# Kernel optimization log

Measured on AMD Instinct MI355X. Metric: run time of the kernel, lower is better.

The kernel has to match this reference:

```python
import jax, jax.numpy as jnp
import numpy as np

N, E, T, IN, H, OUT = 100000, 800000, 8, 3, 32, 64


def _lstm_dir(pre, Whh, bhh, reverse):
    # pre: [T, E, 4H] precomputed input contribution (x @ W_ih^T + b_ih)
    Hh = Whh.shape[1]

    def step(carry, xt):
        h, c = carry
        g = xt + h @ Whh.T + bhh  # [E, 4H], pytorch gate order i,f,g,o
        i = jax.nn.sigmoid(g[:, :Hh])
        f = jax.nn.sigmoid(g[:, Hh:2 * Hh])
        gg = jnp.tanh(g[:, 2 * Hh:3 * Hh])
        o = jax.nn.sigmoid(g[:, 3 * Hh:])
        c = f * c + i * gg
        h = o * jnp.tanh(c)
        return (h, c), None

    init = (jnp.zeros((pre.shape[1], Hh), pre.dtype),
            jnp.zeros((pre.shape[1], Hh), pre.dtype))
    (h, c), _ = jax.lax.scan(step, init, pre, reverse=reverse)
    return c  # final cell state [E, H]


def _mlp(x, W1, W2):
    # MLP(num_layers=2, bias=False): lin1 -> relu -> lin2
    return jax.nn.relu(x @ W1.T) @ W2.T


def setup_inputs() -> dict:
    key = jax.random.key(0)
    ks = jax.random.split(key, 18)
    s = 0.1
    inp = {
        "x": jax.random.normal(ks[0], (N, IN), jnp.float32),
        "edge_traj": jax.random.normal(ks[1], (E, T, 6), jnp.float32),
        "w_ih_f": jax.random.normal(ks[2], (4 * H, 6), jnp.float32) * s,
        "w_hh_f": jax.random.normal(ks[3], (4 * H, H), jnp.float32) * s,
        "b_ih_f": jax.random.normal(ks[4], (4 * H,), jnp.float32) * s,
        "b_hh_f": jax.random.normal(ks[5], (4 * H,), jnp.float32) * s,
        "w_ih_b": jax.random.normal(ks[6], (4 * H, 6), jnp.float32) * s,
        "w_hh_b": jax.random.normal(ks[7], (4 * H, H), jnp.float32) * s,
        "b_ih_b": jax.random.normal(ks[8], (4 * H,), jnp.float32) * s,
        "b_hh_b": jax.random.normal(ks[9], (4 * H,), jnp.float32) * s,
        "coor_w1": jax.random.normal(ks[10], (H, IN), jnp.float32) * s,
        "coor_w2": jax.random.normal(ks[11], (H, H), jnp.float32) * s,
        "nn2_w1": jax.random.normal(ks[12], (H, 3 * H), jnp.float32) * s,
        "nn2_w2": jax.random.normal(ks[13], (H, H), jnp.float32) * s,
        "nn_w1": jax.random.normal(ks[14], (H, H), jnp.float32) * s,
        "nn_w2": jax.random.normal(ks[15], (OUT, H), jnp.float32) * s,
        "edge_index": jax.random.randint(ks[16], (2, E), 0, N, dtype=jnp.int32),
    }
    return inp


def reference(x, edge_traj, w_ih_f, w_hh_f, b_ih_f, b_hh_f,
              w_ih_b, w_hh_b, b_ih_b, b_hh_b,
              coor_w1, coor_w2, nn2_w1, nn2_w2, nn_w1, nn_w2, edge_index):
    # bidirectional 1-layer LSTM over edge trajectories; edge attr = c_t.mean(dim=0)
    pre_f = jnp.einsum('etf,gf->teg', edge_traj, w_ih_f) + b_ih_f
    pre_b = jnp.einsum('etf,gf->teg', edge_traj, w_ih_b) + b_ih_b
    c_f = _lstm_dir(pre_f, w_hh_f, b_hh_f, reverse=False)
    c_b = _lstm_dir(pre_b, w_hh_b, b_hh_b, reverse=True)
    traj_encoding = 0.5 * (c_f + c_b)  # [E, H]

    coor = _mlp(x, coor_w1, coor_w2)  # [N, H]

    src, dst = edge_index[0], edge_index[1]  # flow: source_to_target
    # message: nn2(cat[x_i, x_j, edge_attr]) per edge
    msg_in = jnp.concatenate([coor[dst], coor[src], traj_encoding], axis=-1)  # [E, 3H]
    msg = _mlp(msg_in, nn2_w1, nn2_w2)  # [E, H]
    agg = jax.ops.segment_sum(msg, dst, num_segments=N)  # [N, H]

    out = _mlp(agg, nn_w1, nn_w2)  # [N, OUT]; (note: GINEConv.forward skips (1+eps)*x)
    return out.sum(axis=0)  # [OUT]
```

## Files before the change

### kernel.cpp

```cpp
#include <hip/hip_runtime.h>
#include <hip/hip_bf16.h>

typedef __attribute__((ext_vector_type(8))) short  bf16x8;
typedef __attribute__((ext_vector_type(4))) float  f32x4;

#define MTPW 4
#define LOG2E  1.442695041f
#define LOG2E2 2.885390082f

__device__ __forceinline__ float rcp_(float v){ return __builtin_amdgcn_rcpf(v); }
__device__ __forceinline__ float exp2_(float v){ return __builtin_amdgcn_exp2f(v); }
__device__ __forceinline__ unsigned pk2(float lo, float hi){
    __hip_bfloat162 h = __float22bfloat162_rn(float2{lo, hi});
    return *(unsigned*)&h;
}
__device__ __forceinline__ float lo2f(unsigned u){ return __uint_as_float(u << 16); }
__device__ __forceinline__ float hi2f(unsigned u){ return __uint_as_float(u & 0xFFFF0000u); }

union U4 { bf16x8 v; unsigned u[4]; };

__device__ __forceinline__ bf16x8 ldw8(const float* __restrict__ p){
    const float4 a = *(const float4*)p;
    const float4 b = *(const float4*)(p + 4);
    U4 r;
    r.u[0] = pk2(a.x, a.y); r.u[1] = pk2(a.z, a.w);
    r.u[2] = pk2(b.x, b.y); r.u[3] = pk2(b.z, b.w);
    return r.v;
}
__device__ __forceinline__ bf16x8 ldw8p(const float* __restrict__ rowp, int lq, float s){
    const float4 a = *(const float4*)(rowp + 4*lq);
    const float4 b = *(const float4*)(rowp + 16 + 4*lq);
    U4 r;
    r.u[0] = pk2(a.x*s, a.y*s); r.u[1] = pk2(a.z*s, a.w*s);
    r.u[2] = pk2(b.x*s, b.y*s); r.u[3] = pk2(b.z*s, b.w*s);
    return r.v;
}
__device__ __forceinline__ bf16x8 ldihs(const float* __restrict__ wih,
                                        const float* __restrict__ bi,
                                        const float* __restrict__ bh,
                                        int row, int lq, float s){
    U4 r;
    r.u[0] = r.u[1] = r.u[2] = r.u[3] = 0u;
    if (lq == 0) {
        const float* p = wih + row * 6;
        r.u[0] = pk2(p[0]*s, p[1]*s);
        r.u[1] = pk2(p[2]*s, p[3]*s);
        r.u[2] = pk2(p[4]*s, p[5]*s);
        r.u[3] = pk2((bi[row] + bh[row])*s, 0.0f);
    }
    return r.v;
}

__global__ __launch_bounds__(256) void coor_kernel(
    const float* __restrict__ x, const float* __restrict__ w1,
    const float* __restrict__ w2, unsigned short* __restrict__ coorb, int N)
{
    __shared__ float sW1[96];
    __shared__ float sW2[1024];
    const int tid = threadIdx.x;
    if (tid < 96) sW1[tid] = w1[tid];
    for (int i = tid; i < 1024; i += 256) sW2[i] = w2[i];
    __syncthreads();
    int n = blockIdx.x * 256 + tid;
    if (n >= N) return;
    const float x0 = x[n*3+0], x1 = x[n*3+1], x2 = x[n*3+2];
    float h[32];
#pragma unroll
    for (int k = 0; k < 32; ++k)
        h[k] = fmaxf(sW1[k*3+0]*x0 + sW1[k*3+1]*x1 + sW1[k*3+2]*x2, 0.0f);
    union { uint4 q[4]; unsigned u[16]; } st;
#pragma unroll
    for (int p = 0; p < 16; ++p) {
        float a0 = 0.f, a1 = 0.f;
#pragma unroll
        for (int k = 0; k < 32; ++k) {
            a0 += sW2[(2*p)  *32 + k] * h[k];
            a1 += sW2[(2*p+1)*32 + k] * h[k];
        }
        st.u[p] = pk2(a0, a1);
    }
    uint4* cp = (uint4*)(coorb + (size_t)n * 32);
#pragma unroll
    for (int w = 0; w < 4; ++w) cp[w] = st.q[w];
}

template<int DIR>
__global__ __launch_bounds__(256, 3) void lstm_kernel(
    const float* __restrict__ edge_traj,
    const float* __restrict__ w_ih, const float* __restrict__ w_hh,
    const float* __restrict__ b_ih, const float* __restrict__ b_hh,
    unsigned* __restrict__ cbuf, int E)
{
    const int lane = threadIdx.x & 63;
    const int wid  = threadIdx.x >> 6;
    const int le   = lane & 15;
    const int lq   = lane >> 4;
    const bool l0  = (lq == 0);
    const f32x4 Z4 = {0.f, 0.f, 0.f, 0.f};

    bf16x8 wh[8], wx[8];
#pragma unroll
    for (int m = 0; m < 8; ++m) {
        const int row = 16*m + le;
        const float s = (m == 4 || m == 5) ? LOG2E2 : -LOG2E;
        wh[m] = ldw8p(w_hh + row*32, lq, s);
        wx[m] = ldihs(w_ih, b_ih, b_hh, row, lq, s);
    }

    const long tile = (long)blockIdx.x * 4 + wid;
    const long e0 = tile * 16;
    if (e0 >= E) return;
    const long er = e0 + le;
    const bool valid = er < E;
    const long ec = valid ? er : (E - 1);
    const float* xb = edge_traj + ec * 48;

    U4 hf; hf.u[0] = hf.u[1] = hf.u[2] = hf.u[3] = 0u;
    float cl[4] = {0,0,0,0}, ch[4] = {0,0,0,0};
#pragma unroll
    for (int t = 0; t < 8; ++t) {
        const int te = DIR ? (7 - t) : t;
        U4 xf;
        {
            const float* xp = xb + te * 6;
            const float2 a  = *(const float2*)xp;
            const float2 b2 = *(const float2*)(xp + 2);
            const float2 c2 = *(const float2*)(xp + 4);
            xf.u[0] = l0 ? pk2(a.x, a.y)   : 0u;
            xf.u[1] = l0 ? pk2(b2.x, b2.y) : 0u;
            xf.u[2] = l0 ? pk2(c2.x, c2.y) : 0u;
            xf.u[3] = l0 ? 0x3f80u         : 0u;
        }
        f32x4 acc[8];
#pragma unroll
        for (int m = 0; m < 8; ++m)
            acc[m] = __builtin_amdgcn_mfma_f32_16x16x32_bf16(wx[m], xf.v, Z4, 0, 0, 0);
        if (t > 0) {
#pragma unroll
            for (int m = 0; m < 8; ++m)
                acc[m] = __builtin_amdgcn_mfma_f32_16x16x32_bf16(wh[m], hf.v, acc[m], 0, 0, 0);
        }
        float h_lo[4], h_hi[4];
#pragma unroll
        for (int r = 0; r < 4; ++r) {
            {
                const float Ea = exp2_(acc[0][r]);
                const float Ef = exp2_(acc[2][r]);
                const float Eg = exp2_(acc[4][r]);
                const float Eo = exp2_(acc[6][r]);
                const float p  = (Ea + 1.f) * (Eg + 1.f);
                const float f1 = Ef + 1.f;
                const float num = fmaf(cl[r], p, (Eg - 1.f) * f1);
                cl[r] = num * rcp_(p * f1);
                const float Ec = exp2_(LOG2E2 * cl[r]);
                h_lo[r] = (Ec - 1.f) * rcp_((Eo + 1.f) * (Ec + 1.f));
            }
            {
                const float Ea = exp2_(acc[1][r]);
                const float Ef = exp2_(acc[3][r]);
                const float Eg = exp2_(acc[5][r]);
                const float Eo = exp2_(acc[7][r]);
                const float p  = (Ea + 1.f) * (Eg + 1.f);
                const float f1 = Ef + 1.f;
                const float num = fmaf(ch[r], p, (Eg - 1.f) * f1);
                ch[r] = num * rcp_(p * f1);
                const float Ec = exp2_(LOG2E2 * ch[r]);
                h_hi[r] = (Ec - 1.f) * rcp_((Eo + 1.f) * (Ec + 1.f));
            }
        }
        if (t < 7) {
            hf.u[0] = pk2(h_lo[0], h_lo[1]);
            hf.u[1] = pk2(h_lo[2], h_lo[3]);
            hf.u[2] = pk2(h_hi[0], h_hi[1]);
            hf.u[3] = pk2(h_hi[2], h_hi[3]);
        }
    }

    if (valid) {
        U4 cw;
        cw.u[0] = pk2(cl[0], cl[1]);
        cw.u[1] = pk2(cl[2], cl[3]);
        cw.u[2] = pk2(ch[0], ch[1]);
        cw.u[3] = pk2(ch[2], ch[3]);
        unsigned* dp = cbuf + er * 16 + lq * 4;
        if (DIR == 0) {
            *(uint4*)dp = *(uint4*)cw.u;
        } else {
            const uint4 f = *(const uint4*)dp;
            uint4 o;
            o.x = pk2(0.5f*(lo2f(f.x)+lo2f(cw.u[0])), 0.5f*(hi2f(f.x)+hi2f(cw.u[0])));
            o.y = pk2(0.5f*(lo2f(f.y)+lo2f(cw.u[1])), 0.5f*(hi2f(f.y)+hi2f(cw.u[1])));
            o.z = pk2(0.5f*(lo2f(f.z)+lo2f(cw.u[2])), 0.5f*(hi2f(f.z)+hi2f(cw.u[2])));
            o.w = pk2(0.5f*(lo2f(f.w)+lo2f(cw.u[3])), 0.5f*(hi2f(f.w)+hi2f(cw.u[3])));
            *(uint4*)dp = o;
        }
    }
}

__global__ __launch_bounds__(256, 4) void msg_kernel(
    unsigned* trmsg,
    const float* __restrict__ nn2_w1, const float* __restrict__ nn2_w2,
    const int* __restrict__ edge_index,
    const unsigned short* __restrict__ coorb, int E)
{
    const int lane = threadIdx.x & 63;
    const int wid  = threadIdx.x >> 6;
    const int le   = lane & 15;
    const int lq   = lane >> 4;
    const f32x4 Z4 = {0.f, 0.f, 0.f, 0.f};

    bf16x8 w1a[2][3], w2a[2];
#pragma unroll
    for (int mm = 0; mm < 2; ++mm) {
        const int row = 16*mm + le;
        w1a[mm][0] = ldw8(nn2_w1 + row*96 +  8*lq);
        w1a[mm][1] = ldw8(nn2_w1 + row*96 + 32 + 8*lq);
        w1a[mm][2] = ldw8p(nn2_w1 + row*96 + 64, lq, 1.0f);
        w2a[mm]    = ldw8p(nn2_w2 + row*32, lq, 1.0f);
    }

    const long gw = (long)blockIdx.x * 4 + wid;
    for (int it = 0; it < MTPW; ++it) {
        const long tile = gw * MTPW + it;
        const long e0 = tile * 16;
        if (e0 >= E) break;
        const long e_raw = e0 + le;
        const bool valid = e_raw < E;
        const long ec = valid ? e_raw : (E - 1);

        U4 tf;
        if (valid) *(uint4*)tf.u = *(const uint4*)(trmsg + e_raw * 16 + lq * 4);
        else tf.u[0] = tf.u[1] = tf.u[2] = tf.u[3] = 0u;

        const int src = edge_index[ec];
        const int dst = edge_index[E + ec];
        U4 df, sf;
        {
            const uint4 dv = *(const uint4*)(coorb + (size_t)dst*32 + lq*8);
            const uint4 sv = *(const uint4*)(coorb + (size_t)src*32 + lq*8);
            df.u[0]=dv.x; df.u[1]=dv.y; df.u[2]=dv.z; df.u[3]=dv.w;
            sf.u[0]=sv.x; sf.u[1]=sv.y; sf.u[2]=sv.z; sf.u[3]=sv.w;
        }

        f32x4 h1[2];
#pragma unroll
        for (int mm = 0; mm < 2; ++mm) {
            f32x4 a = __builtin_amdgcn_mfma_f32_16x16x32_bf16(w1a[mm][0], df.v, Z4, 0, 0, 0);
            a = __builtin_amdgcn_mfma_f32_16x16x32_bf16(w1a[mm][1], sf.v, a, 0, 0, 0);
            a = __builtin_amdgcn_mfma_f32_16x16x32_bf16(w1a[mm][2], tf.v, a, 0, 0, 0);
            h1[mm] = a;
        }
        U4 gf;
        gf.u[0] = pk2(fmaxf(h1[0][0],0.f), fmaxf(h1[0][1],0.f));
        gf.u[1] = pk2(fmaxf(h1[0][2],0.f), fmaxf(h1[0][3],0.f));
        gf.u[2] = pk2(fmaxf(h1[1][0],0.f), fmaxf(h1[1][1],0.f));
        gf.u[3] = pk2(fmaxf(h1[1][2],0.f), fmaxf(h1[1][3],0.f));

        const f32x4 o0 = __builtin_amdgcn_mfma_f32_16x16x32_bf16(w2a[0], gf.v, Z4, 0, 0, 0);
        const f32x4 o1 = __builtin_amdgcn_mfma_f32_16x16x32_bf16(w2a[1], gf.v, Z4, 0, 0, 0);
        if (valid) {
            U4 cw;
            cw.u[0] = pk2(o0[0], o0[1]);
            cw.u[1] = pk2(o0[2], o0[3]);
            cw.u[2] = pk2(o1[0], o1[1]);
            cw.u[3] = pk2(o1[2], o1[3]);
            *(uint4*)(trmsg + e_raw * 16 + lq * 4) = *(uint4*)cw.u;
        }
    }
}

__global__ __launch_bounds__(256) void hist_kernel(
    const int* __restrict__ ei, int* __restrict__ cnt, int E)
{
    const int e = blockIdx.x*256 + threadIdx.x;
    if (e < E) atomicAdd(&cnt[ei[E + e]], 1);
}

__global__ __launch_bounds__(256) void scan1_kernel(
    const int* __restrict__ cnt, int* __restrict__ bsum, int N)
{
    __shared__ int sp[4];
    const int tid = threadIdx.x;
    const int n = blockIdx.x*256 + tid;
    int c = (n < N) ? cnt[n] : 0;
#pragma unroll
    for (int m = 1; m < 64; m <<= 1) c += __shfl_xor(c, m, 64);
    if ((tid & 63) == 0) sp[tid >> 6] = c;
    __syncthreads();
    if (tid == 0) bsum[blockIdx.x] = sp[0] + sp[1] + sp[2] + sp[3];
}

__global__ __launch_bounds__(512) void scan2_kernel(
    int* __restrict__ bsum, int* __restrict__ offs, int nblk, int E, int N)
{
    __shared__ int s[512];
    const int tid = threadIdx.x;
    const int v = (tid < nblk) ? bsum[tid] : 0;
    s[tid] = v;
    __syncthreads();
    for (int off = 1; off < 512; off <<= 1) {
        const int t = (tid >= off) ? s[tid - off] : 0;
        __syncthreads();
        s[tid] += t;
        __syncthreads();
    }
    if (tid < nblk) bsum[tid] = s[tid] - v;
    if (tid == 0) offs[N] = E;
}

__global__ __launch_bounds__(256) void scan3_kernel(
    const int* __restrict__ cnt, const int* __restrict__ bsum,
    int* __restrict__ offs, int* __restrict__ cursor, int N)
{
    __shared__ int s[256];
    const int tid = threadIdx.x;
    const int n = blockIdx.x*256 + tid;
    const int v = (n < N) ? cnt[n] : 0;
    s[tid] = v;
    __syncthreads();
    for (int off = 1; off < 256; off <<= 1) {
        const int t = (tid >= off) ? s[tid - off] : 0;
        __syncthreads();
        s[tid] += t;
        __syncthreads();
    }
    if (n < N) {
        const int o = bsum[blockIdx.x] + s[tid] - v;
        offs[n] = o;
        cursor[n] = o;
    }
}

__global__ __launch_bounds__(256) void fill_kernel(
    const int* __restrict__ ei, int* __restrict__ cursor,
    int* __restrict__ eidx, int E)
{
    const int e = blockIdx.x*256 + threadIdx.x;
    if (e < E) {
        const int p = atomicAdd(&cursor[ei[E + e]], 1);
        eidx[p] = e;
    }
}

__global__ __launch_bounds__(256) void gather_kernel(
    const unsigned* __restrict__ msg, const int* __restrict__ offs,
    const int* __restrict__ eidx, float* __restrict__ aggv, int N)
{
    const int lane = threadIdx.x & 63;
    const int wid  = threadIdx.x >> 6;
    const int g  = lane >> 4;
    const int le = lane & 15;
    const int n = blockIdx.x*16 + wid*4 + g;
    if (n >= N) return;
    const int beg = offs[n], end = offs[n+1];
    float sx = 0.f, sy = 0.f;
    for (int i = beg; i < end; ++i) {
        const unsigned w = msg[(size_t)eidx[i]*16 + le];
        sx += lo2f(w); sy += hi2f(w);
    }
    *(float2*)(aggv + (size_t)n*32 + 2*le) = float2{sx, sy};
}

__global__ __launch_bounds__(256) void agg_kernel(
    const float* __restrict__ aggv, const float* __restrict__ nn_w1,
    float* __restrict__ partials, int N)
{
    __shared__ float sW[1024];
    __shared__ float sP[4][32];
    const int tid = threadIdx.x;
    for (int i = tid; i < 1024; i += 256) {
        const int jj = i >> 5, s = i & 31, q = s >> 3, j = s & 7;
        const int col = (j < 4) ? (4*q + j) : (16 + 4*q + (j - 4));
        sW[i] = nn_w1[jj*32 + col];
    }
    __syncthreads();
    const int n = blockIdx.x*256 + tid;
    float h[32];
    if (n < N) {
        float a[32];
        const float4* ap = (const float4*)(aggv + (size_t)n*32);
#pragma unroll
        for (int k4 = 0; k4 < 8; ++k4) {
            const float4 v = ap[k4];
            a[k4*4]=v.x; a[k4*4+1]=v.y; a[k4*4+2]=v.z; a[k4*4+3]=v.w;
        }
#pragma unroll
        for (int jj = 0; jj < 32; ++jj) {
            float acc = 0.f;
#pragma unroll
            for (int k = 0; k < 32; ++k) acc += sW[jj*32+k]*a[k];
            h[jj] = fmaxf(acc, 0.f);
        }
    } else {
#pragma unroll
        for (int jj = 0; jj < 32; ++jj) h[jj] = 0.f;
    }
#pragma unroll
    for (int m = 1; m < 64; m <<= 1) {
#pragma unroll
        for (int k = 0; k < 32; ++k) h[k] += __shfl_xor(h[k], m, 64);
    }
    if ((tid & 63) == 0) {
#pragma unroll
        for (int k = 0; k < 32; ++k) sP[tid >> 6][k] = h[k];
    }
    __syncthreads();
    if (tid < 32)
        partials[(size_t)blockIdx.x * 32 + tid]
            = sP[0][tid] + sP[1][tid] + sP[2][tid] + sP[3][tid];
}

__global__ __launch_bounds__(256) void reduce_kernel(
    const float* __restrict__ partials, const float* __restrict__ nn_w2,
    float* __restrict__ out, int nblk)
{
    __shared__ float sR[8][32];
    __shared__ float sS[32];
    const int tid = threadIdx.x;
    const int col = tid & 31;
    const int row = tid >> 5;
    float s = 0.f;
    for (int i = row; i < nblk; i += 8) s += partials[(size_t)i*32 + col];
    sR[row][col] = s;
    __syncthreads();
    if (row == 0) {
        float t = 0.f;
#pragma unroll
        for (int r = 0; r < 8; ++r) t += sR[r][col];
        sS[col] = t;
    }
    __syncthreads();
    if (tid < 64) {
        float acc = 0.f;
#pragma unroll
        for (int k = 0; k < 32; ++k) acc += nn_w2[tid*32+k] * sS[k];
        out[tid] = acc;
    }
}

extern "C" void kernel_launch(void* const* d_in, const int* in_sizes, int n_in,
                              void* d_out, int out_size, void* d_ws, size_t ws_size,
                              hipStream_t stream)
{
    const float* x         = (const float*)d_in[0];
    const float* edge_traj = (const float*)d_in[1];
    const float* w_ih_f    = (const float*)d_in[2];
    const float* w_hh_f    = (const float*)d_in[3];
    const float* b_ih_f    = (const float*)d_in[4];
    const float* b_hh_f    = (const float*)d_in[5];
    const float* w_ih_b    = (const float*)d_in[6];
    const float* w_hh_b    = (const float*)d_in[7];
    const float* b_ih_b    = (const float*)d_in[8];
    const float* b_hh_b    = (const float*)d_in[9];
    const float* coor_w1   = (const float*)d_in[10];
    const float* coor_w2   = (const float*)d_in[11];
    const float* nn2_w1    = (const float*)d_in[12];
    const float* nn2_w2    = (const float*)d_in[13];
    const float* nn_w1     = (const float*)d_in[14];
    const float* nn_w2     = (const float*)d_in[15];
    const int* edge_index  = (const int*)d_in[16];
    const int N = in_sizes[0] / 3;
    const int E = in_sizes[16] / 2;
    const int nblk = (N + 255) / 256;

    float* aggv = (float*)d_ws;
    float* partials = aggv + (size_t)N * 32;
    unsigned short* coorb = (unsigned short*)(partials + (size_t)nblk * 32);
    unsigned* cbuf = (unsigned*)(coorb + (size_t)N * 32);
    int* cnt    = (int*)(cbuf + (size_t)E * 16);
    int* offs   = cnt + N;
    int* cursor = offs + N + 1;
    int* eidx   = cursor + N;
    int* bsum   = eidx + E;

    (void)hipMemsetAsync(cnt, 0, (size_t)N * sizeof(int), stream);

    coor_kernel<<<nblk, 256, 0, stream>>>(x, coor_w1, coor_w2, coorb, N);

    const long tiles   = ((long)E + 15) / 16;
    const int  lblocks = (int)((tiles + 3) / 4);
    lstm_kernel<0><<<lblocks, 256, 0, stream>>>(edge_traj,
        w_ih_f, w_hh_f, b_ih_f, b_hh_f, cbuf, E);
    lstm_kernel<1><<<lblocks, 256, 0, stream>>>(edge_traj,
        w_ih_b, w_hh_b, b_ih_b, b_hh_b, cbuf, E);

    const int eblk = (E + 255) / 256;
    hist_kernel<<<eblk, 256, 0, stream>>>(edge_index, cnt, E);
    scan1_kernel<<<nblk, 256, 0, stream>>>(cnt, bsum, N);
    scan2_kernel<<<1, 512, 0, stream>>>(bsum, offs, nblk, E, N);
    scan3_kernel<<<nblk, 256, 0, stream>>>(cnt, bsum, offs, cursor, N);
    fill_kernel<<<eblk, 256, 0, stream>>>(edge_index, cursor, eidx, E);

    const int mblocks = (int)((tiles + 4*MTPW - 1) / (4*MTPW));
    msg_kernel<<<mblocks, 256, 0, stream>>>(cbuf, nn2_w1, nn2_w2,
        edge_index, coorb, E);

    gather_kernel<<<(N + 15)/16, 256, 0, stream>>>(cbuf, offs, eidx, aggv, N);
    agg_kernel<<<nblk, 256, 0, stream>>>(aggv, nn_w1, partials, N);
    reduce_kernel<<<1, 256, 0, stream>>>(partials, nn_w2, (float*)d_out, nblk);
}
```

Measured before the change: 720.6 us.

## Stage LSTM weights in LDS and process two edge tiles per wave

```diff
diff --git a/kernel.cpp b/kernel.cpp
--- a/kernel.cpp
+++ b/kernel.cpp
@@ -1,12 +1,14 @@
 #include <hip/hip_runtime.h>
 #include <hip/hip_bf16.h>
 
-typedef __attribute__((ext_vector_type(8))) short  bf16x8;
-typedef __attribute__((ext_vector_type(4))) float  f32x4;
+typedef __attribute__((ext_vector_type(8))) short    bf16x8;
+typedef __attribute__((ext_vector_type(4))) float    f32x4;
+typedef __attribute__((ext_vector_type(4))) unsigned u32x4;
 
 #define MTPW 4
 #define LOG2E  1.442695041f
 #define LOG2E2 2.885390082f
+#define MFMA __builtin_amdgcn_mfma_f32_16x16x32_bf16
 
 __device__ __forceinline__ float rcp_(float v){ return __builtin_amdgcn_rcpf(v); }
 __device__ __forceinline__ float exp2_(float v){ return __builtin_amdgcn_exp2f(v); }
@@ -35,20 +37,39 @@
     r.u[2] = pk2(b.x*s, b.y*s); r.u[3] = pk2(b.z*s, b.w*s);
     return r.v;
 }
-__device__ __forceinline__ bf16x8 ldihs(const float* __restrict__ wih,
-                                        const float* __restrict__ bi,
-                                        const float* __restrict__ bh,
-                                        int row, int lq, float s){
-    U4 r;
-    r.u[0] = r.u[1] = r.u[2] = r.u[3] = 0u;
-    if (lq == 0) {
-        const float* p = wih + row * 6;
-        r.u[0] = pk2(p[0]*s, p[1]*s);
-        r.u[1] = pk2(p[2]*s, p[3]*s);
-        r.u[2] = pk2(p[4]*s, p[5]*s);
-        r.u[3] = pk2((bi[row] + bh[row])*s, 0.0f);
-    }
-    return r.v;
+
+#define LDS_RD8(d0,d1,d2,d3,d4,d5,d6,d7,O0,O1,O2,O3,O4,O5,O6,O7)            \
+  asm volatile("ds_read_b128 %0, %8 offset:" O0 "\n\t"                      \
+               "ds_read_b128 %1, %8 offset:" O1 "\n\t"                      \
+               "ds_read_b128 %2, %8 offset:" O2 "\n\t"                      \
+               "ds_read_b128 %3, %8 offset:" O3 "\n\t"                      \
+               "ds_read_b128 %4, %8 offset:" O4 "\n\t"                      \
+               "ds_read_b128 %5, %8 offset:" O5 "\n\t"                      \
+               "ds_read_b128 %6, %8 offset:" O6 "\n\t"                      \
+               "ds_read_b128 %7, %8 offset:" O7 "\n\t"                      \
+               "s_waitcnt lgkmcnt(0)"                                       \
+               : "=&v"(d0),"=&v"(d1),"=&v"(d2),"=&v"(d3),                   \
+                 "=&v"(d4),"=&v"(d5),"=&v"(d6),"=&v"(d7)                    \
+               : "v"(lds_addr))
+
+__device__ __forceinline__ bf16x8 bc8(u32x4 x){ return __builtin_bit_cast(bf16x8, x); }
+
+__device__ __forceinline__ void gates4(const f32x4 ai, const f32x4 af,
+                                       const f32x4 ag, const f32x4 ao,
+                                       float c[4], float h[4]){
+#pragma unroll
+    for (int r = 0; r < 4; ++r) {
+        const float Ea = exp2_(ai[r]);
+        const float Ef = exp2_(af[r]);
+        const float Eg = exp2_(ag[r]);
+        const float Eo = exp2_(ao[r]);
+        const float p  = (Ea + 1.f) * (Eg + 1.f);
+        const float f1 = Ef + 1.f;
+        const float num = fmaf(c[r], p, (Eg - 1.f) * f1);
+        c[r] = num * rcp_(p * f1);
+        const float Ec = exp2_(LOG2E2 * c[r]);
+        h[r] = (Ec - 1.f) * rcp_((Eo + 1.f) * (Ec + 1.f));
+    }
 }
 
 __global__ __launch_bounds__(256) void coor_kernel(
@@ -85,98 +106,149 @@
 }
 
 template<int DIR>
-__global__ __launch_bounds__(256, 3) void lstm_kernel(
+__global__ __launch_bounds__(256, 2) void lstm_kernel(
     const float* __restrict__ edge_traj,
     const float* __restrict__ w_ih, const float* __restrict__ w_hh,
     const float* __restrict__ b_ih, const float* __restrict__ b_hh,
     unsigned* __restrict__ cbuf, int E)
 {
-    const int lane = threadIdx.x & 63;
-    const int wid  = threadIdx.x >> 6;
+    __shared__ unsigned lds_w[4096];
+    const int tid = threadIdx.x;
+    for (int i = tid; i < 512; i += 256) {
+        const int m = i >> 6, ln = i & 63;
+        const int le2 = ln & 15, lq2 = ln >> 4;
+        const int row = 16*m + le2;
+        const float s = (m == 4 || m == 5) ? LOG2E2 : -LOG2E;
+        const float4 a = *(const float4*)(w_hh + row*32 + 4*lq2);
+        const float4 b = *(const float4*)(w_hh + row*32 + 16 + 4*lq2);
+        unsigned* wp = &lds_w[(size_t)i * 4];
+        wp[0] = pk2(a.x*s, a.y*s); wp[1] = pk2(a.z*s, a.w*s);
+        wp[2] = pk2(b.x*s, b.y*s); wp[3] = pk2(b.z*s, b.w*s);
+        unsigned* xp = &lds_w[(size_t)(512 + i) * 4];
+        if (lq2 == 0) {
+            const float* p = w_ih + row * 6;
+            xp[0] = pk2(p[0]*s, p[1]*s);
+            xp[1] = pk2(p[2]*s, p[3]*s);
+            xp[2] = pk2(p[4]*s, p[5]*s);
+            xp[3] = pk2((b_ih[row] + b_hh[row])*s, 0.f);
+        } else {
+            xp[0] = 0u; xp[1] = 0u; xp[2] = 0u; xp[3] = 0u;
+        }
+    }
+    __syncthreads();
+
+    const int lane = tid & 63;
+    const int wid  = tid >> 6;
     const int le   = lane & 15;
     const int lq   = lane >> 4;
     const bool l0  = (lq == 0);
+    const unsigned lds_addr = (unsigned)(size_t)lds_w + (unsigned)lane * 16u;
     const f32x4 Z4 = {0.f, 0.f, 0.f, 0.f};
 
-    bf16x8 wh[8], wx[8];
-#pragma unroll
-    for (int m = 0; m < 8; ++m) {
-        const int row = 16*m + le;
-        const float s = (m == 4 || m == 5) ? LOG2E2 : -LOG2E;
-        wh[m] = ldw8p(w_hh + row*32, lq, s);
-        wx[m] = ldihs(w_ih, b_ih, b_hh, row, lq, s);
-    }
-
-    const long tile = (long)blockIdx.x * 4 + wid;
-    const long e0 = tile * 16;
+    const long pr = (long)blockIdx.x * 4 + wid;
+    const long e0 = pr * 32;
     if (e0 >= E) return;
-    const long er = e0 + le;
-    const bool valid = er < E;
-    const long ec = valid ? er : (E - 1);
-    const float* xb = edge_traj + ec * 48;
-
-    U4 hf; hf.u[0] = hf.u[1] = hf.u[2] = hf.u[3] = 0u;
-    float cl[4] = {0,0,0,0}, ch[4] = {0,0,0,0};
+    const long eA = e0 + le, eB = e0 + 16 + le;
+    const bool vA = eA < E, vB = eB < E;
+    const float* xbA = edge_traj + (vA ? eA : (E - 1)) * 48;
+    const float* xbB = edge_traj + (vB ? eB : (E - 1)) * 48;
+
+    U4 hfA, hfB;
+    hfA.u[0]=hfA.u[1]=hfA.u[2]=hfA.u[3]=0u;
+    hfB.u[0]=hfB.u[1]=hfB.u[2]=hfB.u[3]=0u;
+    float clA[4]={0,0,0,0}, chA[4]={0,0,0,0};
+    float clB[4]={0,0,0,0}, chB[4]={0,0,0,0};
+
 #pragma unroll
     for (int t = 0; t < 8; ++t) {
         const int te = DIR ? (7 - t) : t;
-        U4 xf;
+        U4 xfA, xfB;
         {
-            const float* xp = xb + te * 6;
+            const float* xp = xbA + te * 6;
             const float2 a  = *(const float2*)xp;
             const float2 b2 = *(const float2*)(xp + 2);
             const float2 c2 = *(const float2*)(xp + 4);
-            xf.u[0] = l0 ? pk2(a.x, a.y)   : 0u;
-            xf.u[1] = l0 ? pk2(b2.x, b2.y) : 0u;
-            xf.u[2] = l0 ? pk2(c2.x, c2.y) : 0u;
-            xf.u[3] = l0 ? 0x3f80u         : 0u;
-        }
-        f32x4 acc[8];
-#pragma unroll
-        for (int m = 0; m < 8; ++m)
-            acc[m] = __builtin_amdgcn_mfma_f32_16x16x32_bf16(wx[m], xf.v, Z4, 0, 0, 0);
+            xfA.u[0] = l0 ? pk2(a.x, a.y)   : 0u;
+            xfA.u[1] = l0 ? pk2(b2.x, b2.y) : 0u;
+            xfA.u[2] = l0 ? pk2(c2.x, c2.y) : 0u;
+            xfA.u[3] = l0 ? 0x3f80u         : 0u;
+        }
+        {
+            const float* xp = xbB + te * 6;
+            const float2 a  = *(const float2*)xp;
+            const float2 b2 = *(const float2*)(xp + 2);
+            const float2 c2 = *(const float2*)(xp + 4);
+            xfB.u[0] = l0 ? pk2(a.x, a.y)   : 0u;
+            xfB.u[1] = l0 ? pk2(b2.x, b2.y) : 0u;
+            xfB.u[2] = l0 ? pk2(c2.x, c2.y) : 0u;
+            xfB.u[3] = l0 ? 0x3f80u         : 0u;
+        }
+
+        u32x4 f0,f1,f2,f3,f4,f5,f6,f7;
+        LDS_RD8(f0,f1,f2,f3,f4,f5,f6,f7,
+                "0","2048","4096","6144","8192","10240","12288","14336");
+        f32x4 aiA = MFMA(bc8(f4), xfA.v, Z4, 0,0,0);
+        f32x4 afA = MFMA(bc8(f5), xfA.v, Z4, 0,0,0);
+        f32x4 agA = MFMA(bc8(f6), xfA.v, Z4, 0,0,0);
+        f32x4 aoA = MFMA(bc8(f7), xfA.v, Z4, 0,0,0);
+        f32x4 aiB = MFMA(bc8(f4), xfB.v, Z4, 0,0,0);
+        f32x4 afB = MFMA(bc8(f5), xfB.v, Z4, 0,0,0);
+        f32x4 agB = MFMA(bc8(f6), xfB.v, Z4, 0,0,0);
+        f32x4 aoB = MFMA(bc8(f7), xfB.v, Z4, 0,0,0);
         if (t > 0) {
-#pragma unroll
-            for (int m = 0; m < 8; ++m)
-                acc[m] = __builtin_amdgcn_mfma_f32_16x16x32_bf16(wh[m], hf.v, acc[m], 0, 0, 0);
-        }
-        float h_lo[4], h_hi[4];
-#pragma unroll
-        for (int r = 0; r < 4; ++r) {
-            {
-                const float Ea = exp2_(acc[0][r]);
-                const float Ef = exp2_(acc[2][r]);
-                const float Eg = exp2_(acc[4][r]);
-                const float Eo = exp2_(acc[6][r]);
-                const float p  = (Ea + 1.f) * (Eg + 1.f);
-                const float f1 = Ef + 1.f;
-                const float num = fmaf(cl[r], p, (Eg - 1.f) * f1);
-                cl[r] = num * rcp_(p * f1);
-                const float Ec = exp2_(LOG2E2 * cl[r]);
-                h_lo[r] = (Ec - 1.f) * rcp_((Eo + 1.f) * (Ec + 1.f));
-            }
-            {
-                const float Ea = exp2_(acc[1][r]);
-                const float Ef = exp2_(acc[3][r]);
-                const float Eg = exp2_(acc[5][r]);
-                const float Eo = exp2_(acc[7][r]);
-                const float p  = (Ea + 1.f) * (Eg + 1.f);
-                const float f1 = Ef + 1.f;
-                const float num = fmaf(ch[r], p, (Eg - 1.f) * f1);
-                ch[r] = num * rcp_(p * f1);
-                const float Ec = exp2_(LOG2E2 * ch[r]);
-                h_hi[r] = (Ec - 1.f) * rcp_((Eo + 1.f) * (Ec + 1.f));
-            }
-        }
+            aiA = MFMA(bc8(f0), hfA.v, aiA, 0,0,0);
+            afA = MFMA(bc8(f1), hfA.v, afA, 0,0,0);
+            agA = MFMA(bc8(f2), hfA.v, agA, 0,0,0);
+            aoA = MFMA(bc8(f3), hfA.v, aoA, 0,0,0);
+            aiB = MFMA(bc8(f0), hfB.v, aiB, 0,0,0);
+            afB = MFMA(bc8(f1), hfB.v, afB, 0,0,0);
+            agB = MFMA(bc8(f2), hfB.v, agB, 0,0,0);
+            aoB = MFMA(bc8(f3), hfB.v, aoB, 0,0,0);
+        }
+        u32x4 g0,g1,g2,g3,g4,g5,g6,g7;
+        LDS_RD8(g0,g1,g2,g3,g4,g5,g6,g7,
+                "1024","3072","5120","7168","9216","11264","13312","15360");
+        float hlA[4], hlB[4];
+        gates4(aiA, afA, agA, aoA, clA, hlA);
+        gates4(aiB, afB, agB, aoB, clB, hlB);
+
+        f32x4 biA = MFMA(bc8(g4), xfA.v, Z4, 0,0,0);
+        f32x4 bfA = MFMA(bc8(g5), xfA.v, Z4, 0,0,0);
+        f32x4 bgA = MFMA(bc8(g6), xfA.v, Z4, 0,0,0);
+        f32x4 boA = MFMA(bc8(g7), xfA.v, Z4, 0,0,0);
+        f32x4 biB = MFMA(bc8(g4), xfB.v, Z4, 0,0,0);
+        f32x4 bfB = MFMA(bc8(g5), xfB.v, Z4, 0,0,0);
+        f32x4 bgB = MFMA(bc8(g6), xfB.v, Z4, 0,0,0);
+        f32x4 boB = MFMA(bc8(g7), xfB.v, Z4, 0,0,0);
+        if (t > 0) {
+            biA = MFMA(bc8(g0), hfA.v, biA, 0,0,0);
+            bfA = MFMA(bc8(g1), hfA.v, bfA, 0,0,0);
+            bgA = MFMA(bc8(g2), hfA.v, bgA, 0,0,0);
+            boA = MFMA(bc8(g3), hfA.v, boA, 0,0,0);
+            biB = MFMA(bc8(g0), hfB.v, biB, 0,0,0);
+            bfB = MFMA(bc8(g1), hfB.v, bfB, 0,0,0);
+            bgB = MFMA(bc8(g2), hfB.v, bgB, 0,0,0);
+            boB = MFMA(bc8(g3), hfB.v, boB, 0,0,0);
+        }
+        float hhA[4], hhB[4];
+        gates4(biA, bfA, bgA, boA, chA, hhA);
+        gates4(biB, bfB, bgB, boB, chB, hhB);
+
         if (t < 7) {
-            hf.u[0] = pk2(h_lo[0], h_lo[1]);
-            hf.u[1] = pk2(h_lo[2], h_lo[3]);
-            hf.u[2] = pk2(h_hi[0], h_hi[1]);
-            hf.u[3] = pk2(h_hi[2], h_hi[3]);
-        }
-    }
-
-    if (valid) {
+            hfA.u[0] = pk2(hlA[0], hlA[1]); hfA.u[1] = pk2(hlA[2], hlA[3]);
+            hfA.u[2] = pk2(hhA[0], hhA[1]); hfA.u[3] = pk2(hhA[2], hhA[3]);
+            hfB.u[0] = pk2(hlB[0], hlB[1]); hfB.u[1] = pk2(hlB[2], hlB[3]);
+            hfB.u[2] = pk2(hhB[0], hhB[1]); hfB.u[3] = pk2(hhB[2], hhB[3]);
+        }
+    }
+
+#pragma unroll
+    for (int p = 0; p < 2; ++p) {
+        const float* cl = p ? clB : clA;
+        const float* ch = p ? chB : chA;
+        const bool  vst = p ? vB : vA;
+        const long  er  = p ? eB : eA;
+        if (!vst) continue;
         U4 cw;
         cw.u[0] = pk2(cl[0], cl[1]);
         cw.u[1] = pk2(cl[2], cl[3]);
@@ -245,9 +317,9 @@
         f32x4 h1[2];
 #pragma unroll
         for (int mm = 0; mm < 2; ++mm) {
-            f32x4 a = __builtin_amdgcn_mfma_f32_16x16x32_bf16(w1a[mm][0], df.v, Z4, 0, 0, 0);
-            a = __builtin_amdgcn_mfma_f32_16x16x32_bf16(w1a[mm][1], sf.v, a, 0, 0, 0);
-            a = __builtin_amdgcn_mfma_f32_16x16x32_bf16(w1a[mm][2], tf.v, a, 0, 0, 0);
+            f32x4 a = MFMA(w1a[mm][0], df.v, Z4, 0,0,0);
+            a = MFMA(w1a[mm][1], sf.v, a, 0,0,0);
+            a = MFMA(w1a[mm][2], tf.v, a, 0,0,0);
             h1[mm] = a;
         }
         U4 gf;
@@ -256,8 +328,8 @@
         gf.u[2] = pk2(fmaxf(h1[1][0],0.f), fmaxf(h1[1][1],0.f));
         gf.u[3] = pk2(fmaxf(h1[1][2],0.f), fmaxf(h1[1][3],0.f));
 
-        const f32x4 o0 = __builtin_amdgcn_mfma_f32_16x16x32_bf16(w2a[0], gf.v, Z4, 0, 0, 0);
-        const f32x4 o1 = __builtin_amdgcn_mfma_f32_16x16x32_bf16(w2a[1], gf.v, Z4, 0, 0, 0);
+        const f32x4 o0 = MFMA(w2a[0], gf.v, Z4, 0,0,0);
+        const f32x4 o1 = MFMA(w2a[1], gf.v, Z4, 0,0,0);
         if (valid) {
             U4 cw;
             cw.u[0] = pk2(o0[0], o0[1]);
@@ -478,7 +550,8 @@
     coor_kernel<<<nblk, 256, 0, stream>>>(x, coor_w1, coor_w2, coorb, N);
 
     const long tiles   = ((long)E + 15) / 16;
-    const int  lblocks = (int)((tiles + 3) / 4);
+    const long pairs   = (tiles + 1) / 2;
+    const int  lblocks = (int)((pairs + 3) / 4);
     lstm_kernel<0><<<lblocks, 256, 0, stream>>>(edge_traj,
         w_ih_f, w_hh_f, b_ih_f, b_hh_f, cbuf, E);
     lstm_kernel<1><<<lblocks, 256, 0, stream>>>(edge_traj,
```

Result: faster. 653.3 us (-9.3%).
